# Kernel tuning notes

Hardware: AMD Instinct MI355X
Metric: run time of the kernel (lower is better)

Reference implementation:

```python
import jax, jax.numpy as jnp
import numpy as np

D = 256  # input_dim


def setup_inputs() -> dict:
    key = jax.random.key(0)
    ks = jax.random.split(key, 10)
    s = 1.0 / np.sqrt(D)  # torch Linear init scale (uniform bound)
    desc0 = jax.random.normal(ks[0], (4, 4096, D), dtype=jnp.float32)
    desc1 = jax.random.normal(ks[1], (4, 4096, D), dtype=jnp.float32)
    def lin(kw, kb):
        W = jax.random.uniform(kw, (D, D), jnp.float32, -s, s)
        b = jax.random.uniform(kb, (D,), jnp.float32, -s, s)
        return W, b
    Wq, bq = lin(ks[2], ks[3])
    Wk, bk = lin(ks[4], ks[5])
    Wv, bv = lin(ks[6], ks[7])
    Wo, bo = lin(ks[8], ks[9])
    return {"desc0": desc0, "desc1": desc1,
            "Wq": Wq, "bq": bq, "Wk": Wk, "bk": bk,
            "Wv": Wv, "bv": bv, "Wo": Wo, "bo": bo}


def reference(desc0, desc1, Wq, bq, Wk, bk, Wv, bv, Wo, bo):
    # torch Linear: y = x @ W.T + b
    q = desc0 @ Wq.T + bq                      # [B, N0, D]
    k = desc1 @ Wk.T + bk                      # [B, N1, D]
    v = desc1 @ Wv.T + bv                      # [B, N1, D]
    scale = 1.0 / jnp.sqrt(jnp.asarray(q.shape[-1], q.dtype))
    attn = jnp.einsum('bqd,bkd->bqk', q, k) * scale  # [B, N0, N1]
    weights = jax.nn.softmax(attn, axis=-1)
    out = jnp.einsum('bqk,bkd->bqd', weights, v)     # [B, N0, D]
    return out @ Wo.T + bo
```

## Files before the change

kernel.cpp:

```cpp
#include <hip/hip_runtime.h>


typedef __attribute__((ext_vector_type(8))) __bf16 bf16x8;
typedef __attribute__((ext_vector_type(4))) float f32x4;
typedef __attribute__((ext_vector_type(16))) float f32x16;
typedef __attribute__((ext_vector_type(4))) unsigned int u32x4;
typedef __attribute__((ext_vector_type(2))) unsigned int u32x2;
typedef __attribute__((ext_vector_type(4))) unsigned short us16x4;

__device__ __forceinline__ unsigned short f2bf(float f) {
  unsigned u = __builtin_bit_cast(unsigned, f);
  u += 0x7FFFu + ((u >> 16) & 1u);
  return (unsigned short)(u >> 16);
}
__device__ __forceinline__ unsigned pk2(float a, float b) {
  return (unsigned)f2bf(a) | ((unsigned)f2bf(b) << 16);
}
__device__ __forceinline__ unsigned cvtpk(float lo, float hi) {
  unsigned r;
  asm("v_cvt_pk_bf16_f32 %0, %1, %2" : "=v"(r) : "v"(lo), "v"(hi));
  return r;
}
__device__ __forceinline__ float bf2f(unsigned short s) {
  return __builtin_bit_cast(float, ((unsigned)s) << 16);
}
__device__ __forceinline__ int swz4(int r) { return (r ^ (r >> 2)) & 3; }
__device__ __forceinline__ bf16x8 ldbf16(const void* p) {
  return __builtin_bit_cast(bf16x8, *(const u32x4*)p);
}
__device__ __forceinline__ f32x4 mfma16(bf16x8 a, bf16x8 b, f32x4 c) {
  return __builtin_amdgcn_mfma_f32_16x16x32_bf16(a, b, c, 0, 0, 0);
}
__device__ __forceinline__ f32x16 mfma32(bf16x8 a, bf16x8 b, f32x16 c) {
  return __builtin_amdgcn_mfma_f32_32x32x16_bf16(a, b, c, 0, 0, 0);
}
__device__ __forceinline__ void gld16(void* lds, const void* gsrc) {
  __builtin_amdgcn_global_load_lds(
      (const __attribute__((address_space(1))) unsigned int*)gsrc,
      (__attribute__((address_space(3))) unsigned int*)lds, 16, 0, 0);
}

template <int IN_MODE, int MODE>
__global__ __launch_bounds__(256, 4) void proj_k(const void* __restrict__ Ain,
                                                 const float* __restrict__ W,
                                                 const float* __restrict__ bias,
                                                 void* __restrict__ Cout,
                                                 const float* __restrict__ lwA) {
  __shared__ __align__(16) unsigned short Al[2][64 * 32];
  __shared__ __align__(16) unsigned short Wl[2][64 * 32];
  __shared__ float biasl[64];
  const int tid = threadIdx.x;
  const int w = tid >> 6, l = tid & 63, g = l >> 4, c = l & 15;
  const int mt = blockIdx.x & 255, nq = blockIdx.x >> 8;
  const int row0 = mt * 64, n0 = nq * 64;
  if (tid < 64) biasl[tid] = bias[n0 + tid];

  const int sr = tid >> 2, seg = tid & 3;
  const int ssw = swz4(sr);

  float ainv = 1.f;
  if (IN_MODE >= 2) {
    const int grow = row0 + sr;
    float lt = lwA[grow];
    if (IN_MODE == 2) lt += lwA[16384 + grow];
    ainv = 1.f / lt;
  }

  {
    if (IN_MODE == 1) {
      const unsigned short* ap = (const unsigned short*)Ain + (size_t)(row0 + sr) * 256 + seg * 8;
      *(u32x4*)&Al[0][sr * 32 + ((seg ^ ssw) << 3)] = *(const u32x4*)ap;
    } else if (IN_MODE >= 2) {
      const unsigned short* ap = (const unsigned short*)Ain + (size_t)(row0 + sr) * 256 + seg * 8;
      u32x4 a0 = *(const u32x4*)ap, v;
      u32x4 a1 = (IN_MODE == 2) ? *(const u32x4*)(ap + 4194304) : a0;
#pragma unroll
      for (int i = 0; i < 4; ++i) {
        float lo = bf2f((unsigned short)(a0[i] & 0xFFFF));
        float hi = bf2f((unsigned short)(a0[i] >> 16));
        if (IN_MODE == 2) {
          lo += bf2f((unsigned short)(a1[i] & 0xFFFF));
          hi += bf2f((unsigned short)(a1[i] >> 16));
        }
        v[i] = pk2(lo * ainv, hi * ainv);
      }
      *(u32x4*)&Al[0][sr * 32 + ((seg ^ ssw) << 3)] = v;
    } else {
      const float* ap = (const float*)Ain + (size_t)(row0 + sr) * 256 + seg * 8;
      float4 x = *(const float4*)ap, y = *(const float4*)(ap + 4);
      u32x4 v; v[0] = pk2(x.x, x.y); v[1] = pk2(x.z, x.w); v[2] = pk2(y.x, y.y); v[3] = pk2(y.z, y.w);
      *(u32x4*)&Al[0][sr * 32 + ((seg ^ ssw) << 3)] = v;
    }
    const float* wp = W + (size_t)(n0 + sr) * 256 + seg * 8;
    float4 x = *(const float4*)wp, y = *(const float4*)(wp + 4);
    u32x4 v; v[0] = pk2(x.x, x.y); v[1] = pk2(x.z, x.w); v[2] = pk2(y.x, y.y); v[3] = pk2(y.z, y.w);
    *(u32x4*)&Wl[0][sr * 32 + ((seg ^ ssw) << 3)] = v;
  }
  __syncthreads();

  f32x4 acc[4];
#pragma unroll
  for (int jt = 0; jt < 4; ++jt) acc[jt] = (f32x4){0.f, 0.f, 0.f, 0.f};

#pragma unroll 1
  for (int ch = 0; ch < 8; ++ch) {
    const int cur = ch & 1;
    const bool pre = (ch + 1 < 8);
    float4 ax, ay, wx, wy; u32x4 abv, abv2;
    if (pre) {
      const int ko = (ch + 1) * 32 + seg * 8;
      if (IN_MODE == 1) {
        abv = *(const u32x4*)((const unsigned short*)Ain + (size_t)(row0 + sr) * 256 + ko);
      } else if (IN_MODE >= 2) {
        const unsigned short* ap = (const unsigned short*)Ain + (size_t)(row0 + sr) * 256 + ko;
        abv = *(const u32x4*)ap;
        if (IN_MODE == 2) abv2 = *(const u32x4*)(ap + 4194304);
      } else {
        const float* ap = (const float*)Ain + (size_t)(row0 + sr) * 256 + ko;
        ax = *(const float4*)ap; ay = *(const float4*)(ap + 4);
      }
      const float* wp = W + (size_t)(n0 + sr) * 256 + ko;
      wx = *(const float4*)wp; wy = *(const float4*)(wp + 4);
    }
    const int ra = w * 16 + c;
    bf16x8 af = ldbf16(&Al[cur][ra * 32 + ((g ^ swz4(ra)) << 3)]);
#pragma unroll
    for (int jt = 0; jt < 4; ++jt) {
      const int j = jt * 16 + c;
      bf16x8 bfr = ldbf16(&Wl[cur][j * 32 + ((g ^ swz4(j)) << 3)]);
      acc[jt] = mfma16(af, bfr, acc[jt]);
    }
    if (pre) {
      u32x4 v;
      if (IN_MODE == 1) v = abv;
      else if (IN_MODE >= 2) {
#pragma unroll
        for (int i = 0; i < 4; ++i) {
          float lo = bf2f((unsigned short)(abv[i] & 0xFFFF));
          float hi = bf2f((unsigned short)(abv[i] >> 16));
          if (IN_MODE == 2) {
            lo += bf2f((unsigned short)(abv2[i] & 0xFFFF));
            hi += bf2f((unsigned short)(abv2[i] >> 16));
          }
          v[i] = pk2(lo * ainv, hi * ainv);
        }
      } else {
        v[0] = pk2(ax.x, ax.y); v[1] = pk2(ax.z, ax.w); v[2] = pk2(ay.x, ay.y); v[3] = pk2(ay.z, ay.w);
      }
      *(u32x4*)&Al[1 - cur][sr * 32 + ((seg ^ ssw) << 3)] = v;
      u32x4 vw; vw[0] = pk2(wx.x, wx.y); vw[1] = pk2(wx.z, wx.w); vw[2] = pk2(wy.x, wy.y); vw[3] = pk2(wy.z, wy.w);
      *(u32x4*)&Wl[1 - cur][sr * 32 + ((seg ^ ssw) << 3)] = vw;
    }
    __syncthreads();
  }

#pragma unroll
  for (int jt = 0; jt < 4; ++jt) {
    const int col = n0 + jt * 16 + c;
    const float bv = biasl[jt * 16 + c];
    const int rloc = w * 16 + (g << 2);
    if (MODE == 0) {
      unsigned short* q = (unsigned short*)Cout;
#pragma unroll
      for (int r = 0; r < 4; ++r)
        q[(size_t)(row0 + rloc + r) * 256 + col] = f2bf(acc[jt][r] + bv);
    } else if (MODE == 1) {
      unsigned short* vt = (unsigned short*)Cout;
      const int n = row0 + rloc;
      const int b = n >> 12, nl = n & 4095;
      us16x4 pk;
      pk[0] = f2bf(acc[jt][0] + bv); pk[1] = f2bf(acc[jt][1] + bv);
      pk[2] = f2bf(acc[jt][2] + bv); pk[3] = f2bf(acc[jt][3] + bv);
      *(us16x4*)(vt + (size_t)b * 1048576 + (size_t)(nl >> 6) * 16384 + col * 64 + (nl & 63)) = pk;
    } else {
      float* o = (float*)Cout;
#pragma unroll
      for (int r = 0; r < 4; ++r)
        o[(size_t)(row0 + rloc + r) * 256 + col] = acc[jt][r] + bv;
    }
  }
}

template <int NS>
__global__ __launch_bounds__(512, 2) void attn_k(const unsigned short* __restrict__ qg,
                                                 const unsigned short* __restrict__ kg,
                                                 const unsigned short* __restrict__ vg,
                                                 unsigned short* __restrict__ part,
                                                 float* __restrict__ lw) {
  __shared__ __align__(16) unsigned char smem[148480];
  const int tid = threadIdx.x, w = tid >> 6, l = tid & 63;
  const int l31 = l & 31, h5 = l >> 5;
  const int qt = w >> 1, hf = w & 1;
  const int dh = w >> 1, qh = w & 1;
  const int bid = blockIdx.x;
  const int b4 = bid & 3;
  const int s = (NS == 2) ? ((bid >> 2) & 1) : 0;
  const int qtl = (NS == 2) ? (bid >> 3) : (bid >> 2);
  const int q0 = qtl * 128;
  const int NT = (NS == 2) ? 32 : 64;

  const unsigned short* kb = kg + (size_t)b4 * 1048576 + (size_t)s * 524288;
  const unsigned short* vb = vg + (size_t)b4 * 1048576 + (size_t)s * 32 * 16384;

  bf16x8 qf[16];
  {
    const unsigned short* qp = qg + ((size_t)b4 * 4096 + q0 + qt * 32 + l31) * 256;
#pragma unroll
    for (int kst = 0; kst < 16; ++kst) qf[kst] = ldbf16(qp + kst * 16 + h5 * 8);
  }

  f32x16 o[4];
#pragma unroll
  for (int d = 0; d < 4; ++d)
#pragma unroll
    for (int r = 0; r < 16; ++r) o[d][r] = 0.f;
  float l_run = 0.f;

  int goffK[4], goffV[4];
#pragma unroll
  for (int i = 0; i < 4; ++i) {
    const int sl = i * 512 + tid;
    const int kk = sl >> 5, ch = sl & 31;
    goffK[i] = kk * 256 + ((ch ^ (kk & 31)) << 3);
    const int r = sl >> 4, p16 = sl & 15;
    const int x = p16 ^ (r & 15);
    goffV[i] = (2 * r + (x >> 3)) * 64 + ((x & 7) << 3);
  }
#define STAGE(buf, t1)                                                                   \
  {                                                                                      \
    const unsigned short* _ks = kb + (size_t)(t1) * 16384;                               \
    const unsigned short* _vs = vb + (size_t)(t1) * 16384;                               \
    _Pragma("unroll") for (int i = 0; i < 4; ++i)                                        \
        gld16(smem + (buf) * 32768 + i * 8192 + w * 1024, _ks + goffK[i]);               \
    _Pragma("unroll") for (int i = 0; i < 4; ++i)                                        \
        gld16(smem + 65536 + (buf) * 32768 + i * 8192 + w * 1024, _vs + goffV[i]);       \
  }

  STAGE(0, 0);
  __syncthreads();

  const float alpha = 0.09016844f;
  unsigned char* Pq = smem + 131072 + qt * 4096;
  const int kkr = hf * 32 + l31;

#pragma unroll 1
  for (int t = 0; t < NT; ++t) {
    const int cur = t & 1;
    if (t + 1 < NT) STAGE(1 - cur, t + 1);

    const unsigned char* Kc = smem + cur * 32768 + kkr * 512;
    f32x16 sa, sb;
#pragma unroll
    for (int r = 0; r < 16; ++r) { sa[r] = 0.f; sb[r] = 0.f; }
    __builtin_amdgcn_s_setprio(1);
#pragma unroll
    for (int kst = 0; kst < 16; ++kst) {
      bf16x8 kf = ldbf16(Kc + (((kst * 2 + h5) ^ l31) << 4));
      if (kst & 1) sb = mfma32(kf, qf[kst], sb);
      else         sa = mfma32(kf, qf[kst], sa);
    }
    __builtin_amdgcn_s_setprio(0);

    float p[16];
#pragma unroll
    for (int r = 0; r < 16; ++r) p[r] = exp2f((sa[r] + sb[r]) * alpha);
    float ls = ((p[0] + p[1]) + (p[2] + p[3])) + ((p[4] + p[5]) + (p[6] + p[7])) +
               (((p[8] + p[9]) + (p[10] + p[11])) + ((p[12] + p[13]) + (p[14] + p[15])));
    ls += __shfl_xor(ls, 32);
    l_run += ls;

    unsigned u[8];
#pragma unroll
    for (int i = 0; i < 8; ++i) u[i] = cvtpk(p[2 * i], p[2 * i + 1]);
#pragma unroll
    for (int j = 0; j < 4; ++j) {
      u32x2 dv; dv[0] = u[2 * j]; dv[1] = u[2 * j + 1];
      *(u32x2*)(Pq + l31 * 128 + (((j + 4 * hf) ^ (l31 & 7)) << 4) + h5 * 8) = dv;
    }

    asm volatile("s_waitcnt lgkmcnt(0)\n\ts_barrier" ::: "memory");
    __builtin_amdgcn_sched_barrier(0);

    const unsigned char* Vc = smem + 65536 + cur * 32768;
    bf16x8 va[8];
#pragma unroll
    for (int dd = 0; dd < 2; ++dd) {
      const int dm = dh * 64 + dd * 32 + l31;
      const int rr = dm >> 1;
      const unsigned char* Vr = Vc + rr * 256;
      const int xb = (dm & 1) * 8;
#pragma unroll
      for (int kst = 0; kst < 4; ++kst)
        va[dd * 4 + kst] = ldbf16(Vr + (((xb + kst * 2 + h5) ^ (rr & 15)) << 4));
    }
    __builtin_amdgcn_s_setprio(1);
#pragma unroll
    for (int qq = 0; qq < 2; ++qq) {
      const unsigned char* Pr = smem + 131072 + (qh * 2 + qq) * 4096;
      bf16x8 pb[4];
#pragma unroll
      for (int kst = 0; kst < 4; ++kst)
        pb[kst] = ldbf16(Pr + l31 * 128 + (((kst * 2 + h5) ^ (l31 & 7)) << 4));
#pragma unroll
      for (int dd = 0; dd < 2; ++dd)
#pragma unroll
        for (int kst = 0; kst < 4; ++kst)
          o[dd * 2 + qq] = mfma32(va[dd * 4 + kst], pb[kst], o[dd * 2 + qq]);
    }
    __builtin_amdgcn_s_setprio(0);

    __syncthreads();
  }
#undef STAGE

  float* Lb = (float*)(smem + 147456);
  if (l < 32) Lb[(qt * 2 + hf) * 32 + l31] = l_run;
  __syncthreads();

  unsigned char* T = smem + w * 16384;
#pragma unroll
  for (int dd = 0; dd < 2; ++dd)
#pragma unroll
    for (int qq = 0; qq < 2; ++qq)
#pragma unroll
      for (int rg = 0; rg < 4; ++rg) {
        f32x4 wv;
        wv[0] = o[dd * 2 + qq][4 * rg + 0]; wv[1] = o[dd * 2 + qq][4 * rg + 1];
        wv[2] = o[dd * 2 + qq][4 * rg + 2]; wv[3] = o[dd * 2 + qq][4 * rg + 3];
        const int qloc = qq * 32 + l31;
        const int c16 = dd * 8 + rg * 2 + h5;
        *(f32x4*)(T + qloc * 256 + ((c16 ^ (qloc & 15)) << 4)) = wv;
      }
  asm volatile("s_waitcnt lgkmcnt(0)" ::: "memory");
  __builtin_amdgcn_sched_barrier(0);
  {
    const int qloc = l;
    f32x4 rv[16];
#pragma unroll
    for (int c16 = 0; c16 < 16; ++c16)
      rv[c16] = *(const f32x4*)(T + qloc * 256 + ((c16 ^ (qloc & 15)) << 4));
    unsigned short* op = part + (size_t)s * 4194304 +
                         ((size_t)b4 * 4096 + q0 + qh * 64 + qloc) * 256 + dh * 64;
#pragma unroll
    for (int i = 0; i < 8; ++i) {
      u32x4 ov;
      ov[0] = pk2(rv[2 * i][0], rv[2 * i][1]);
      ov[1] = pk2(rv[2 * i][2], rv[2 * i][3]);
      ov[2] = pk2(rv[2 * i + 1][0], rv[2 * i + 1][1]);
      ov[3] = pk2(rv[2 * i + 1][2], rv[2 * i + 1][3]);
      *(u32x4*)(op + i * 8) = ov;
    }
  }
  if (hf == 0 && l < 32) {
    const float lt = Lb[(qt * 2) * 32 + l31] + Lb[(qt * 2 + 1) * 32 + l31];
    lw[(size_t)s * 16384 + (size_t)b4 * 4096 + q0 + qt * 32 + l31] = lt;
  }
}

extern "C" void kernel_launch(void* const* d_in, const int* in_sizes, int n_in,
                              void* d_out, int out_size, void* d_ws, size_t ws_size,
                              hipStream_t stream) {
  (void)in_sizes; (void)n_in; (void)out_size;
  const float* desc0 = (const float*)d_in[0];
  const float* desc1 = (const float*)d_in[1];
  const float* Wq = (const float*)d_in[2];
  const float* bq = (const float*)d_in[3];
  const float* Wk = (const float*)d_in[4];
  const float* bk = (const float*)d_in[5];
  const float* Wv = (const float*)d_in[6];
  const float* bv = (const float*)d_in[7];
  const float* Wo = (const float*)d_in[8];
  const float* bo = (const float*)d_in[9];

  unsigned char* ws = (unsigned char*)d_ws;
  unsigned short* qw = (unsigned short*)(ws);
  unsigned short* kw = (unsigned short*)(ws + 8388608);
  unsigned short* vw = (unsigned short*)(ws + 16777216);
  unsigned short* part = (unsigned short*)(ws + 25165824);
  float* lwp = (float*)(ws + 41943040);

  const bool two = (ws_size >= 42008576ull);

  proj_k<0, 0><<<1024, 256, 0, stream>>>(desc0, Wq, bq, qw, nullptr);
  proj_k<0, 0><<<1024, 256, 0, stream>>>(desc1, Wk, bk, kw, nullptr);
  proj_k<0, 1><<<1024, 256, 0, stream>>>(desc1, Wv, bv, vw, nullptr);
  if (two) {
    attn_k<2><<<256, 512, 0, stream>>>(qw, kw, vw, part, lwp);
    proj_k<2, 2><<<1024, 256, 0, stream>>>(part, Wo, bo, (float*)d_out, lwp);
  } else {
    lwp = (float*)(ws + 33554432);
    attn_k<1><<<128, 512, 0, stream>>>(qw, kw, vw, part, lwp);
    proj_k<3, 2><<<1024, 256, 0, stream>>>(part, Wo, bo, (float*)d_out, lwp);
  }
}
```

Before: 132.5 us.

## Pre-convert weights to bf16 and compute full-width 64x256 projection tiles per block

Adds a small kernel that converts all four weight matrices to bf16 once, so each projection block streams bf16 weights through async global-to-LDS loads instead of converting fp32 weights itself. Each projection block now covers 64 rows by all 256 output columns with 512 threads, so the A tile is loaded and converted once rather than four times across column blocks. The epilogue writes packed vector stores, using swapped MFMA operands for the row-major outputs. The changes cost an extra launch, a larger LDS footprint per block, and the removal of the LDS swizzle, which may cause bank conflicts.

```diff
diff --git a/kernel.cpp b/kernel.cpp
--- a/kernel.cpp
+++ b/kernel.cpp
@@ -24,7 +24,6 @@
 __device__ __forceinline__ float bf2f(unsigned short s) {
   return __builtin_bit_cast(float, ((unsigned)s) << 16);
 }
-__device__ __forceinline__ int swz4(int r) { return (r ^ (r >> 2)) & 3; }
 __device__ __forceinline__ bf16x8 ldbf16(const void* p) {
   return __builtin_bit_cast(bf16x8, *(const u32x4*)p);
 }
@@ -40,145 +39,160 @@
       (__attribute__((address_space(3))) unsigned int*)lds, 16, 0, 0);
 }
 
+__global__ __launch_bounds__(256, 8) void wconv_k(const float* __restrict__ w0,
+                                                  const float* __restrict__ w1,
+                                                  const float* __restrict__ w2,
+                                                  const float* __restrict__ w3,
+                                                  unsigned short* __restrict__ out) {
+  const int b = blockIdx.x, t = threadIdx.x;
+  const int wi = b >> 5;
+  const float* src = wi == 0 ? w0 : wi == 1 ? w1 : wi == 2 ? w2 : w3;
+  const int idx = ((b & 31) * 256 + t) * 8;
+  float4 x = *(const float4*)(src + idx), y = *(const float4*)(src + idx + 4);
+  u32x4 v;
+  v[0] = pk2(x.x, x.y); v[1] = pk2(x.z, x.w);
+  v[2] = pk2(y.x, y.y); v[3] = pk2(y.z, y.w);
+  *(u32x4*)(out + (size_t)wi * 65536 + idx) = v;
+}
+
 template <int IN_MODE, int MODE>
-__global__ __launch_bounds__(256, 4) void proj_k(const void* __restrict__ Ain,
-                                                 const float* __restrict__ W,
+__global__ __launch_bounds__(512, 2) void proj_k(const void* __restrict__ Ain,
+                                                 const unsigned short* __restrict__ Wb,
                                                  const float* __restrict__ bias,
                                                  void* __restrict__ Cout,
                                                  const float* __restrict__ lwA) {
   __shared__ __align__(16) unsigned short Al[2][64 * 32];
-  __shared__ __align__(16) unsigned short Wl[2][64 * 32];
-  __shared__ float biasl[64];
-  const int tid = threadIdx.x;
-  const int w = tid >> 6, l = tid & 63, g = l >> 4, c = l & 15;
-  const int mt = blockIdx.x & 255, nq = blockIdx.x >> 8;
-  const int row0 = mt * 64, n0 = nq * 64;
-  if (tid < 64) biasl[tid] = bias[n0 + tid];
-
-  const int sr = tid >> 2, seg = tid & 3;
-  const int ssw = swz4(sr);
-
+  __shared__ __align__(16) unsigned short Wl[2][256 * 32];
+  __shared__ float biasl[256];
+  const int tid = threadIdx.x, w = tid >> 6, l = tid & 63, g = l >> 4, c = l & 15;
+  const int rt = w >> 1, ch2 = w & 1;
+  const int row0 = blockIdx.x * 64;
+  if (tid < 256) biasl[tid] = bias[tid];
+
+  const int arow = tid >> 3, aseg = tid & 7;
+  const int agrow = row0 + arow;
   float ainv = 1.f;
   if (IN_MODE >= 2) {
-    const int grow = row0 + sr;
-    float lt = lwA[grow];
-    if (IN_MODE == 2) lt += lwA[16384 + grow];
+    float lt = lwA[agrow];
+    if (IN_MODE == 2) lt += lwA[16384 + agrow];
     ainv = 1.f / lt;
   }
 
+#define STAGEW(buf, ch1)                                                            \
+  {                                                                                 \
+    gld16((unsigned char*)Wl[buf] + tid * 16,                                       \
+          Wb + (tid >> 2) * 256 + (ch1) * 32 + (tid & 3) * 8);                      \
+    gld16((unsigned char*)Wl[buf] + (tid + 512) * 16,                               \
+          Wb + ((tid + 512) >> 2) * 256 + (ch1) * 32 + (tid & 3) * 8);              \
+  }
+#define ACONV(dst, A4, M0, M1)                                                      \
+  {                                                                                 \
+    u32x2 _v;                                                                       \
+    if (IN_MODE == 0) { _v[0] = pk2((A4).x, (A4).y); _v[1] = pk2((A4).z, (A4).w); } \
+    else {                                                                          \
+      float _e0 = bf2f((unsigned short)((M0)[0] & 0xFFFF));                         \
+      float _e1 = bf2f((unsigned short)((M0)[0] >> 16));                            \
+      float _e2 = bf2f((unsigned short)((M0)[1] & 0xFFFF));                         \
+      float _e3 = bf2f((unsigned short)((M0)[1] >> 16));                            \
+      if (IN_MODE == 2) {                                                           \
+        _e0 += bf2f((unsigned short)((M1)[0] & 0xFFFF));                            \
+        _e1 += bf2f((unsigned short)((M1)[0] >> 16));                               \
+        _e2 += bf2f((unsigned short)((M1)[1] & 0xFFFF));                            \
+        _e3 += bf2f((unsigned short)((M1)[1] >> 16));                               \
+      }                                                                             \
+      _v[0] = pk2(_e0 * ainv, _e1 * ainv); _v[1] = pk2(_e2 * ainv, _e3 * ainv);     \
+    }                                                                               \
+    *(u32x2*)(dst) = _v;                                                            \
+  }
+
   {
-    if (IN_MODE == 1) {
-      const unsigned short* ap = (const unsigned short*)Ain + (size_t)(row0 + sr) * 256 + seg * 8;
-      *(u32x4*)&Al[0][sr * 32 + ((seg ^ ssw) << 3)] = *(const u32x4*)ap;
-    } else if (IN_MODE >= 2) {
-      const unsigned short* ap = (const unsigned short*)Ain + (size_t)(row0 + sr) * 256 + seg * 8;
-      u32x4 a0 = *(const u32x4*)ap, v;
-      u32x4 a1 = (IN_MODE == 2) ? *(const u32x4*)(ap + 4194304) : a0;
-#pragma unroll
-      for (int i = 0; i < 4; ++i) {
-        float lo = bf2f((unsigned short)(a0[i] & 0xFFFF));
-        float hi = bf2f((unsigned short)(a0[i] >> 16));
-        if (IN_MODE == 2) {
-          lo += bf2f((unsigned short)(a1[i] & 0xFFFF));
-          hi += bf2f((unsigned short)(a1[i] >> 16));
-        }
-        v[i] = pk2(lo * ainv, hi * ainv);
-      }
-      *(u32x4*)&Al[0][sr * 32 + ((seg ^ ssw) << 3)] = v;
+    STAGEW(0, 0);
+    float4 a4; u32x2 m0, m1;
+    if (IN_MODE == 0) {
+      a4 = *(const float4*)((const float*)Ain + (size_t)agrow * 256 + aseg * 4);
     } else {
-      const float* ap = (const float*)Ain + (size_t)(row0 + sr) * 256 + seg * 8;
-      float4 x = *(const float4*)ap, y = *(const float4*)(ap + 4);
-      u32x4 v; v[0] = pk2(x.x, x.y); v[1] = pk2(x.z, x.w); v[2] = pk2(y.x, y.y); v[3] = pk2(y.z, y.w);
-      *(u32x4*)&Al[0][sr * 32 + ((seg ^ ssw) << 3)] = v;
-    }
-    const float* wp = W + (size_t)(n0 + sr) * 256 + seg * 8;
-    float4 x = *(const float4*)wp, y = *(const float4*)(wp + 4);
-    u32x4 v; v[0] = pk2(x.x, x.y); v[1] = pk2(x.z, x.w); v[2] = pk2(y.x, y.y); v[3] = pk2(y.z, y.w);
-    *(u32x4*)&Wl[0][sr * 32 + ((seg ^ ssw) << 3)] = v;
-  }
-  __syncthreads();
-
-  f32x4 acc[4];
-#pragma unroll
-  for (int jt = 0; jt < 4; ++jt) acc[jt] = (f32x4){0.f, 0.f, 0.f, 0.f};
+      const unsigned short* p0 = (const unsigned short*)Ain + (size_t)agrow * 256 + aseg * 4;
+      m0 = *(const u32x2*)p0;
+      if (IN_MODE == 2) m1 = *(const u32x2*)(p0 + 4194304);
+    }
+    ACONV(&Al[0][arow * 32 + aseg * 4], a4, m0, m1);
+    __syncthreads();
+  }
+
+  f32x4 acc[8];
+#pragma unroll
+  for (int ct = 0; ct < 8; ++ct) acc[ct] = (f32x4){0.f, 0.f, 0.f, 0.f};
 
 #pragma unroll 1
   for (int ch = 0; ch < 8; ++ch) {
     const int cur = ch & 1;
     const bool pre = (ch + 1 < 8);
-    float4 ax, ay, wx, wy; u32x4 abv, abv2;
+    float4 a4; u32x2 m0, m1;
     if (pre) {
-      const int ko = (ch + 1) * 32 + seg * 8;
-      if (IN_MODE == 1) {
-        abv = *(const u32x4*)((const unsigned short*)Ain + (size_t)(row0 + sr) * 256 + ko);
-      } else if (IN_MODE >= 2) {
-        const unsigned short* ap = (const unsigned short*)Ain + (size_t)(row0 + sr) * 256 + ko;
-        abv = *(const u32x4*)ap;
-        if (IN_MODE == 2) abv2 = *(const u32x4*)(ap + 4194304);
+      const int ko = (ch + 1) * 32 + aseg * 4;
+      if (IN_MODE == 0) {
+        a4 = *(const float4*)((const float*)Ain + (size_t)agrow * 256 + ko);
       } else {
-        const float* ap = (const float*)Ain + (size_t)(row0 + sr) * 256 + ko;
-        ax = *(const float4*)ap; ay = *(const float4*)(ap + 4);
+        const unsigned short* p0 = (const unsigned short*)Ain + (size_t)agrow * 256 + ko;
+        m0 = *(const u32x2*)p0;
+        if (IN_MODE == 2) m1 = *(const u32x2*)(p0 + 4194304);
       }
-      const float* wp = W + (size_t)(n0 + sr) * 256 + ko;
-      wx = *(const float4*)wp; wy = *(const float4*)(wp + 4);
-    }
-    const int ra = w * 16 + c;
-    bf16x8 af = ldbf16(&Al[cur][ra * 32 + ((g ^ swz4(ra)) << 3)]);
-#pragma unroll
-    for (int jt = 0; jt < 4; ++jt) {
-      const int j = jt * 16 + c;
-      bf16x8 bfr = ldbf16(&Wl[cur][j * 32 + ((g ^ swz4(j)) << 3)]);
-      acc[jt] = mfma16(af, bfr, acc[jt]);
-    }
-    if (pre) {
-      u32x4 v;
-      if (IN_MODE == 1) v = abv;
-      else if (IN_MODE >= 2) {
-#pragma unroll
-        for (int i = 0; i < 4; ++i) {
-          float lo = bf2f((unsigned short)(abv[i] & 0xFFFF));
-          float hi = bf2f((unsigned short)(abv[i] >> 16));
-          if (IN_MODE == 2) {
-            lo += bf2f((unsigned short)(abv2[i] & 0xFFFF));
-            hi += bf2f((unsigned short)(abv2[i] >> 16));
-          }
-          v[i] = pk2(lo * ainv, hi * ainv);
-        }
-      } else {
-        v[0] = pk2(ax.x, ax.y); v[1] = pk2(ax.z, ax.w); v[2] = pk2(ay.x, ay.y); v[3] = pk2(ay.z, ay.w);
-      }
-      *(u32x4*)&Al[1 - cur][sr * 32 + ((seg ^ ssw) << 3)] = v;
-      u32x4 vw; vw[0] = pk2(wx.x, wx.y); vw[1] = pk2(wx.z, wx.w); vw[2] = pk2(wy.x, wy.y); vw[3] = pk2(wy.z, wy.w);
-      *(u32x4*)&Wl[1 - cur][sr * 32 + ((seg ^ ssw) << 3)] = vw;
-    }
+      STAGEW(1 - cur, ch + 1);
+    }
+    bf16x8 af = ldbf16(&Al[cur][(rt * 16 + c) * 32 + g * 8]);
+#pragma unroll
+    for (int ct = 0; ct < 8; ++ct) {
+      const int j = ch2 * 128 + ct * 16 + c;
+      bf16x8 wf = ldbf16(&Wl[cur][j * 32 + g * 8]);
+      if (MODE == 1) acc[ct] = mfma16(af, wf, acc[ct]);
+      else           acc[ct] = mfma16(wf, af, acc[ct]);
+    }
+    if (pre) ACONV(&Al[1 - cur][arow * 32 + aseg * 4], a4, m0, m1);
     __syncthreads();
   }
 
-#pragma unroll
-  for (int jt = 0; jt < 4; ++jt) {
-    const int col = n0 + jt * 16 + c;
-    const float bv = biasl[jt * 16 + c];
-    const int rloc = w * 16 + (g << 2);
-    if (MODE == 0) {
-      unsigned short* q = (unsigned short*)Cout;
-#pragma unroll
-      for (int r = 0; r < 4; ++r)
-        q[(size_t)(row0 + rloc + r) * 256 + col] = f2bf(acc[jt][r] + bv);
-    } else if (MODE == 1) {
-      unsigned short* vt = (unsigned short*)Cout;
-      const int n = row0 + rloc;
-      const int b = n >> 12, nl = n & 4095;
+  if (MODE == 1) {
+    unsigned short* vt = (unsigned short*)Cout;
+    const int b = row0 >> 12, nb = (row0 & 4095) >> 6;
+    const int nloc = rt * 16 + g * 4;
+#pragma unroll
+    for (int ct = 0; ct < 8; ++ct) {
+      const int col = ch2 * 128 + ct * 16 + c;
+      const float bv = biasl[col];
       us16x4 pk;
-      pk[0] = f2bf(acc[jt][0] + bv); pk[1] = f2bf(acc[jt][1] + bv);
-      pk[2] = f2bf(acc[jt][2] + bv); pk[3] = f2bf(acc[jt][3] + bv);
-      *(us16x4*)(vt + (size_t)b * 1048576 + (size_t)(nl >> 6) * 16384 + col * 64 + (nl & 63)) = pk;
-    } else {
-      float* o = (float*)Cout;
-#pragma unroll
-      for (int r = 0; r < 4; ++r)
-        o[(size_t)(row0 + rloc + r) * 256 + col] = acc[jt][r] + bv;
-    }
-  }
+      pk[0] = f2bf(acc[ct][0] + bv); pk[1] = f2bf(acc[ct][1] + bv);
+      pk[2] = f2bf(acc[ct][2] + bv); pk[3] = f2bf(acc[ct][3] + bv);
+      *(us16x4*)(vt + (size_t)b * 1048576 + (size_t)nb * 16384 + col * 64 + nloc) = pk;
+    }
+  } else if (MODE == 0) {
+    unsigned short* q = (unsigned short*)Cout;
+    const int row = row0 + rt * 16 + c;
+#pragma unroll
+    for (int ct = 0; ct < 8; ++ct) {
+      const int col = ch2 * 128 + ct * 16 + g * 4;
+      us16x4 pk;
+      pk[0] = f2bf(acc[ct][0] + biasl[col + 0]);
+      pk[1] = f2bf(acc[ct][1] + biasl[col + 1]);
+      pk[2] = f2bf(acc[ct][2] + biasl[col + 2]);
+      pk[3] = f2bf(acc[ct][3] + biasl[col + 3]);
+      *(us16x4*)(q + (size_t)row * 256 + col) = pk;
+    }
+  } else {
+    float* o = (float*)Cout;
+    const int row = row0 + rt * 16 + c;
+#pragma unroll
+    for (int ct = 0; ct < 8; ++ct) {
+      const int col = ch2 * 128 + ct * 16 + g * 4;
+      float4 ov;
+      ov.x = acc[ct][0] + biasl[col + 0];
+      ov.y = acc[ct][1] + biasl[col + 1];
+      ov.z = acc[ct][2] + biasl[col + 2];
+      ov.w = acc[ct][3] + biasl[col + 3];
+      *(float4*)(o + (size_t)row * 256 + col) = ov;
+    }
+  }
+#undef STAGEW
+#undef ACONV
 }
 
 template <int NS>
@@ -377,19 +391,27 @@
   unsigned short* kw = (unsigned short*)(ws + 8388608);
   unsigned short* vw = (unsigned short*)(ws + 16777216);
   unsigned short* part = (unsigned short*)(ws + 25165824);
-  float* lwp = (float*)(ws + 41943040);
-
-  const bool two = (ws_size >= 42008576ull);
-
-  proj_k<0, 0><<<1024, 256, 0, stream>>>(desc0, Wq, bq, qw, nullptr);
-  proj_k<0, 0><<<1024, 256, 0, stream>>>(desc1, Wk, bk, kw, nullptr);
-  proj_k<0, 1><<<1024, 256, 0, stream>>>(desc1, Wv, bv, vw, nullptr);
+
+  const bool two = (ws_size >= 42598400ull);
+  float* lwp;
+  unsigned short* wbf;
+  if (two) {
+    lwp = (float*)(ws + 41943040);
+    wbf = (unsigned short*)(ws + 42074112);
+  } else {
+    lwp = (float*)(ws + 33554432);
+    wbf = (unsigned short*)(ws + 33685504);
+  }
+
+  wconv_k<<<128, 256, 0, stream>>>(Wq, Wk, Wv, Wo, wbf);
+  proj_k<0, 0><<<256, 512, 0, stream>>>(desc0, wbf + 0 * 65536, bq, qw, nullptr);
+  proj_k<0, 0><<<256, 512, 0, stream>>>(desc1, wbf + 1 * 65536, bk, kw, nullptr);
+  proj_k<0, 1><<<256, 512, 0, stream>>>(desc1, wbf + 2 * 65536, bv, vw, nullptr);
   if (two) {
     attn_k<2><<<256, 512, 0, stream>>>(qw, kw, vw, part, lwp);
-    proj_k<2, 2><<<1024, 256, 0, stream>>>(part, Wo, bo, (float*)d_out, lwp);
+    proj_k<2, 2><<<256, 512, 0, stream>>>(part, wbf + 3 * 65536, bo, (float*)d_out, lwp);
   } else {
-    lwp = (float*)(ws + 33554432);
     attn_k<1><<<128, 512, 0, stream>>>(qw, kw, vw, part, lwp);
-    proj_k<3, 2><<<1024, 256, 0, stream>>>(part, Wo, bo, (float*)d_out, lwp);
-  }
-}
+    proj_k<3, 2><<<256, 512, 0, stream>>>(part, wbf + 3 * 65536, bo, (float*)d_out, lwp);
+  }
+}
```

Measured after the change: 138.7 us. 1.05x slower.

## Split attention warps into QK producer and PV consumer roles with skewed pipeline

Applied to the files above, without the earlier changes.

The attention kernel now gives its warps two roles. Four warps compute QK scores and exponentials for a 32-key tile, and four warps run the P·V MFMAs for the previous tile one step behind. K tiles are double-buffered, V tiles triple-buffered and P double-buffered in shared memory, with the key tile halved and the tile count doubled. The aim is to overlap softmax math with PV tensor work and drop the mid-iteration barrier. In exchange, consumer warps hold twice the accumulator registers and the unused IN_MODE==1 paths are removed from the projection kernel.

```diff
diff --git a/kernel.cpp b/kernel.cpp
--- a/kernel.cpp
+++ b/kernel.cpp
@@ -67,10 +67,7 @@
   }
 
   {
-    if (IN_MODE == 1) {
-      const unsigned short* ap = (const unsigned short*)Ain + (size_t)(row0 + sr) * 256 + seg * 8;
-      *(u32x4*)&Al[0][sr * 32 + ((seg ^ ssw) << 3)] = *(const u32x4*)ap;
-    } else if (IN_MODE >= 2) {
+    if (IN_MODE >= 2) {
       const unsigned short* ap = (const unsigned short*)Ain + (size_t)(row0 + sr) * 256 + seg * 8;
       u32x4 a0 = *(const u32x4*)ap, v;
       u32x4 a1 = (IN_MODE == 2) ? *(const u32x4*)(ap + 4194304) : a0;
@@ -109,9 +106,7 @@
     float4 ax, ay, wx, wy; u32x4 abv, abv2;
     if (pre) {
       const int ko = (ch + 1) * 32 + seg * 8;
-      if (IN_MODE == 1) {
-        abv = *(const u32x4*)((const unsigned short*)Ain + (size_t)(row0 + sr) * 256 + ko);
-      } else if (IN_MODE >= 2) {
+      if (IN_MODE >= 2) {
         const unsigned short* ap = (const unsigned short*)Ain + (size_t)(row0 + sr) * 256 + ko;
         abv = *(const u32x4*)ap;
         if (IN_MODE == 2) abv2 = *(const u32x4*)(ap + 4194304);
@@ -132,8 +127,7 @@
     }
     if (pre) {
       u32x4 v;
-      if (IN_MODE == 1) v = abv;
-      else if (IN_MODE >= 2) {
+      if (IN_MODE >= 2) {
 #pragma unroll
         for (int i = 0; i < 4; ++i) {
           float lo = bf2f((unsigned short)(abv[i] & 0xFFFF));
@@ -187,173 +181,168 @@
                                                  const unsigned short* __restrict__ vg,
                                                  unsigned short* __restrict__ part,
                                                  float* __restrict__ lw) {
-  __shared__ __align__(16) unsigned char smem[148480];
+  __shared__ __align__(16) unsigned char smem[131072];
   const int tid = threadIdx.x, w = tid >> 6, l = tid & 63;
   const int l31 = l & 31, h5 = l >> 5;
-  const int qt = w >> 1, hf = w & 1;
-  const int dh = w >> 1, qh = w & 1;
+  const bool prod = (w < 4);
+  const int role = w & 3;
   const int bid = blockIdx.x;
   const int b4 = bid & 3;
   const int s = (NS == 2) ? ((bid >> 2) & 1) : 0;
   const int qtl = (NS == 2) ? (bid >> 3) : (bid >> 2);
   const int q0 = qtl * 128;
-  const int NT = (NS == 2) ? 32 : 64;
+  const int NT = (NS == 2) ? 64 : 128;
 
   const unsigned short* kb = kg + (size_t)b4 * 1048576 + (size_t)s * 524288;
   const unsigned short* vb = vg + (size_t)b4 * 1048576 + (size_t)s * 32 * 16384;
 
   bf16x8 qf[16];
-  {
-    const unsigned short* qp = qg + ((size_t)b4 * 4096 + q0 + qt * 32 + l31) * 256;
+  if (prod) {
+    const unsigned short* qp = qg + ((size_t)b4 * 4096 + q0 + role * 32 + l31) * 256;
 #pragma unroll
     for (int kst = 0; kst < 16; ++kst) qf[kst] = ldbf16(qp + kst * 16 + h5 * 8);
   }
-
-  f32x16 o[4];
-#pragma unroll
-  for (int d = 0; d < 4; ++d)
-#pragma unroll
-    for (int r = 0; r < 16; ++r) o[d][r] = 0.f;
+  f32x16 o[8];
+  if (!prod) {
+#pragma unroll
+    for (int i = 0; i < 8; ++i)
+#pragma unroll
+      for (int r = 0; r < 16; ++r) o[i][r] = 0.f;
+  }
   float l_run = 0.f;
 
-  int goffK[4], goffV[4];
-#pragma unroll
-  for (int i = 0; i < 4; ++i) {
+  int gK[2], gV[2];
+#pragma unroll
+  for (int i = 0; i < 2; ++i) {
     const int sl = i * 512 + tid;
     const int kk = sl >> 5, ch = sl & 31;
-    goffK[i] = kk * 256 + ((ch ^ (kk & 31)) << 3);
-    const int r = sl >> 4, p16 = sl & 15;
-    const int x = p16 ^ (r & 15);
-    goffV[i] = (2 * r + (x >> 3)) * 64 + ((x & 7) << 3);
-  }
-#define STAGE(buf, t1)                                                                   \
-  {                                                                                      \
-    const unsigned short* _ks = kb + (size_t)(t1) * 16384;                               \
-    const unsigned short* _vs = vb + (size_t)(t1) * 16384;                               \
-    _Pragma("unroll") for (int i = 0; i < 4; ++i)                                        \
-        gld16(smem + (buf) * 32768 + i * 8192 + w * 1024, _ks + goffK[i]);               \
-    _Pragma("unroll") for (int i = 0; i < 4; ++i)                                        \
-        gld16(smem + 65536 + (buf) * 32768 + i * 8192 + w * 1024, _vs + goffV[i]);       \
-  }
-
-  STAGE(0, 0);
+    gK[i] = kk * 256 + ((ch ^ kk) << 3);
+    const int rr = sl >> 3, cc = (sl & 7) ^ (rr & 7);
+    gV[i] = (rr * 2 + (cc >> 2)) * 64 + ((cc & 3) << 3);
+  }
+#define STAGE(t1)                                                                   \
+  {                                                                                 \
+    const int _t = (t1);                                                            \
+    const unsigned short* _ks = kb + (size_t)_t * 8192;                             \
+    const unsigned short* _vs = vb + (size_t)(_t >> 1) * 16384 + (_t & 1) * 32;     \
+    unsigned char* _kd = smem + (_t & 1) * 16384;                                   \
+    unsigned char* _vd = smem + 32768 + (_t % 3) * 16384;                           \
+    _Pragma("unroll") for (int i = 0; i < 2; ++i)                                   \
+        gld16(_kd + (i * 512 + tid) * 16, _ks + gK[i]);                             \
+    _Pragma("unroll") for (int i = 0; i < 2; ++i)                                   \
+        gld16(_vd + (i * 512 + tid) * 16, _vs + gV[i]);                             \
+  }
+#define PVSTEP(tm1)                                                                 \
+  {                                                                                 \
+    const unsigned char* Vc = smem + 32768 + ((tm1) % 3) * 16384;                   \
+    const unsigned char* Pc = smem + 81920 + ((tm1) & 1) * 8192;                    \
+    bf16x8 va[4];                                                                   \
+    _Pragma("unroll") for (int dd = 0; dd < 2; ++dd) {                              \
+      const int dm = role * 64 + dd * 32 + l31;                                     \
+      const int rr = dm >> 1;                                                       \
+      _Pragma("unroll") for (int kst = 0; kst < 2; ++kst)                           \
+          va[dd * 2 + kst] = ldbf16(Vc + rr * 128 +                                 \
+              ((((dm & 1) * 4 + kst * 2 + h5) ^ (rr & 7)) << 4));                   \
+    }                                                                               \
+    __builtin_amdgcn_s_setprio(1);                                                  \
+    _Pragma("unroll") for (int qq = 0; qq < 4; ++qq) {                              \
+      const unsigned char* Pr = Pc + qq * 2048 + l31 * 64;                          \
+      bf16x8 pb0 = ldbf16(Pr + (((0 + h5) ^ (l31 & 3)) << 4));                      \
+      bf16x8 pb1 = ldbf16(Pr + (((2 + h5) ^ (l31 & 3)) << 4));                      \
+      _Pragma("unroll") for (int dd = 0; dd < 2; ++dd) {                            \
+        o[dd * 4 + qq] = mfma32(va[dd * 2 + 0], pb0, o[dd * 4 + qq]);               \
+        o[dd * 4 + qq] = mfma32(va[dd * 2 + 1], pb1, o[dd * 4 + qq]);               \
+      }                                                                             \
+    }                                                                               \
+    __builtin_amdgcn_s_setprio(0);                                                  \
+  }
+
+  STAGE(0);
   __syncthreads();
 
   const float alpha = 0.09016844f;
-  unsigned char* Pq = smem + 131072 + qt * 4096;
-  const int kkr = hf * 32 + l31;
 
 #pragma unroll 1
   for (int t = 0; t < NT; ++t) {
-    const int cur = t & 1;
-    if (t + 1 < NT) STAGE(1 - cur, t + 1);
-
-    const unsigned char* Kc = smem + cur * 32768 + kkr * 512;
-    f32x16 sa, sb;
-#pragma unroll
-    for (int r = 0; r < 16; ++r) { sa[r] = 0.f; sb[r] = 0.f; }
-    __builtin_amdgcn_s_setprio(1);
-#pragma unroll
-    for (int kst = 0; kst < 16; ++kst) {
-      bf16x8 kf = ldbf16(Kc + (((kst * 2 + h5) ^ l31) << 4));
-      if (kst & 1) sb = mfma32(kf, qf[kst], sb);
-      else         sa = mfma32(kf, qf[kst], sa);
-    }
-    __builtin_amdgcn_s_setprio(0);
-
-    float p[16];
-#pragma unroll
-    for (int r = 0; r < 16; ++r) p[r] = exp2f((sa[r] + sb[r]) * alpha);
-    float ls = ((p[0] + p[1]) + (p[2] + p[3])) + ((p[4] + p[5]) + (p[6] + p[7])) +
-               (((p[8] + p[9]) + (p[10] + p[11])) + ((p[12] + p[13]) + (p[14] + p[15])));
-    ls += __shfl_xor(ls, 32);
-    l_run += ls;
-
-    unsigned u[8];
-#pragma unroll
-    for (int i = 0; i < 8; ++i) u[i] = cvtpk(p[2 * i], p[2 * i + 1]);
-#pragma unroll
-    for (int j = 0; j < 4; ++j) {
-      u32x2 dv; dv[0] = u[2 * j]; dv[1] = u[2 * j + 1];
-      *(u32x2*)(Pq + l31 * 128 + (((j + 4 * hf) ^ (l31 & 7)) << 4) + h5 * 8) = dv;
-    }
-
-    asm volatile("s_waitcnt lgkmcnt(0)\n\ts_barrier" ::: "memory");
+    if (t + 1 < NT) STAGE(t + 1);
+    if (prod) {
+      const unsigned char* Kc = smem + (t & 1) * 16384 + l31 * 512;
+      f32x16 sa, sb;
+#pragma unroll
+      for (int r = 0; r < 16; ++r) { sa[r] = 0.f; sb[r] = 0.f; }
+      __builtin_amdgcn_s_setprio(1);
+#pragma unroll
+      for (int kst = 0; kst < 16; ++kst) {
+        bf16x8 kf = ldbf16(Kc + (((kst * 2 + h5) ^ l31) << 4));
+        if (kst & 1) sb = mfma32(kf, qf[kst], sb);
+        else         sa = mfma32(kf, qf[kst], sa);
+      }
+      __builtin_amdgcn_s_setprio(0);
+      float p[16];
+#pragma unroll
+      for (int r = 0; r < 16; ++r) p[r] = exp2f((sa[r] + sb[r]) * alpha);
+      float ls = ((p[0] + p[1]) + (p[2] + p[3])) + ((p[4] + p[5]) + (p[6] + p[7])) +
+                 (((p[8] + p[9]) + (p[10] + p[11])) + ((p[12] + p[13]) + (p[14] + p[15])));
+      ls += __shfl_xor(ls, 32);
+      l_run += ls;
+      unsigned u[8];
+#pragma unroll
+      for (int i = 0; i < 8; ++i) u[i] = cvtpk(p[2 * i], p[2 * i + 1]);
+      unsigned char* Pq = smem + 81920 + (t & 1) * 8192 + role * 2048 + l31 * 64;
+#pragma unroll
+      for (int j = 0; j < 4; ++j) {
+        u32x2 dv; dv[0] = u[2 * j]; dv[1] = u[2 * j + 1];
+        *(u32x2*)(Pq + ((j ^ (l31 & 3)) << 4) + h5 * 8) = dv;
+      }
+    } else if (t > 0) {
+      PVSTEP(t - 1);
+    }
+    __syncthreads();
+  }
+  if (!prod) PVSTEP(NT - 1);
+#undef STAGE
+#undef PVSTEP
+
+  if (prod && l < 32)
+    lw[(size_t)s * 16384 + (size_t)b4 * 4096 + q0 + role * 32 + l31] = l_run;
+  __syncthreads();
+
+  if (!prod) {
+    unsigned char* T = smem + role * 32768;
+#pragma unroll
+    for (int dd = 0; dd < 2; ++dd)
+#pragma unroll
+      for (int qq = 0; qq < 4; ++qq)
+#pragma unroll
+        for (int rg = 0; rg < 4; ++rg) {
+          f32x4 wv;
+          wv[0] = o[dd * 4 + qq][4 * rg + 0]; wv[1] = o[dd * 4 + qq][4 * rg + 1];
+          wv[2] = o[dd * 4 + qq][4 * rg + 2]; wv[3] = o[dd * 4 + qq][4 * rg + 3];
+          const int qr = qq * 32 + l31;
+          const int c16 = dd * 8 + rg * 2 + h5;
+          *(f32x4*)(T + qr * 256 + ((c16 ^ (qr & 15)) << 4)) = wv;
+        }
+    asm volatile("s_waitcnt lgkmcnt(0)" ::: "memory");
     __builtin_amdgcn_sched_barrier(0);
-
-    const unsigned char* Vc = smem + 65536 + cur * 32768;
-    bf16x8 va[8];
-#pragma unroll
-    for (int dd = 0; dd < 2; ++dd) {
-      const int dm = dh * 64 + dd * 32 + l31;
-      const int rr = dm >> 1;
-      const unsigned char* Vr = Vc + rr * 256;
-      const int xb = (dm & 1) * 8;
-#pragma unroll
-      for (int kst = 0; kst < 4; ++kst)
-        va[dd * 4 + kst] = ldbf16(Vr + (((xb + kst * 2 + h5) ^ (rr & 15)) << 4));
-    }
-    __builtin_amdgcn_s_setprio(1);
-#pragma unroll
-    for (int qq = 0; qq < 2; ++qq) {
-      const unsigned char* Pr = smem + 131072 + (qh * 2 + qq) * 4096;
-      bf16x8 pb[4];
-#pragma unroll
-      for (int kst = 0; kst < 4; ++kst)
-        pb[kst] = ldbf16(Pr + l31 * 128 + (((kst * 2 + h5) ^ (l31 & 7)) << 4));
-#pragma unroll
-      for (int dd = 0; dd < 2; ++dd)
-#pragma unroll
-        for (int kst = 0; kst < 4; ++kst)
-          o[dd * 2 + qq] = mfma32(va[dd * 4 + kst], pb[kst], o[dd * 2 + qq]);
-    }
-    __builtin_amdgcn_s_setprio(0);
-
-    __syncthreads();
-  }
-#undef STAGE
-
-  float* Lb = (float*)(smem + 147456);
-  if (l < 32) Lb[(qt * 2 + hf) * 32 + l31] = l_run;
-  __syncthreads();
-
-  unsigned char* T = smem + w * 16384;
-#pragma unroll
-  for (int dd = 0; dd < 2; ++dd)
-#pragma unroll
-    for (int qq = 0; qq < 2; ++qq)
-#pragma unroll
-      for (int rg = 0; rg < 4; ++rg) {
-        f32x4 wv;
-        wv[0] = o[dd * 2 + qq][4 * rg + 0]; wv[1] = o[dd * 2 + qq][4 * rg + 1];
-        wv[2] = o[dd * 2 + qq][4 * rg + 2]; wv[3] = o[dd * 2 + qq][4 * rg + 3];
-        const int qloc = qq * 32 + l31;
-        const int c16 = dd * 8 + rg * 2 + h5;
-        *(f32x4*)(T + qloc * 256 + ((c16 ^ (qloc & 15)) << 4)) = wv;
-      }
-  asm volatile("s_waitcnt lgkmcnt(0)" ::: "memory");
-  __builtin_amdgcn_sched_barrier(0);
-  {
-    const int qloc = l;
-    f32x4 rv[16];
-#pragma unroll
-    for (int c16 = 0; c16 < 16; ++c16)
-      rv[c16] = *(const f32x4*)(T + qloc * 256 + ((c16 ^ (qloc & 15)) << 4));
-    unsigned short* op = part + (size_t)s * 4194304 +
-                         ((size_t)b4 * 4096 + q0 + qh * 64 + qloc) * 256 + dh * 64;
-#pragma unroll
-    for (int i = 0; i < 8; ++i) {
-      u32x4 ov;
-      ov[0] = pk2(rv[2 * i][0], rv[2 * i][1]);
-      ov[1] = pk2(rv[2 * i][2], rv[2 * i][3]);
-      ov[2] = pk2(rv[2 * i + 1][0], rv[2 * i + 1][1]);
-      ov[3] = pk2(rv[2 * i + 1][2], rv[2 * i + 1][3]);
-      *(u32x4*)(op + i * 8) = ov;
-    }
-  }
-  if (hf == 0 && l < 32) {
-    const float lt = Lb[(qt * 2) * 32 + l31] + Lb[(qt * 2 + 1) * 32 + l31];
-    lw[(size_t)s * 16384 + (size_t)b4 * 4096 + q0 + qt * 32 + l31] = lt;
+#pragma unroll
+    for (int half = 0; half < 2; ++half) {
+      const int qr = half * 64 + l;
+      f32x4 rv[16];
+#pragma unroll
+      for (int c16 = 0; c16 < 16; ++c16)
+        rv[c16] = *(const f32x4*)(T + qr * 256 + ((c16 ^ (qr & 15)) << 4));
+      unsigned short* op = part + (size_t)s * 4194304 +
+                           ((size_t)b4 * 4096 + q0 + qr) * 256 + role * 64;
+#pragma unroll
+      for (int i = 0; i < 8; ++i) {
+        u32x4 ov;
+        ov[0] = pk2(rv[2 * i][0], rv[2 * i][1]);
+        ov[1] = pk2(rv[2 * i][2], rv[2 * i][3]);
+        ov[2] = pk2(rv[2 * i + 1][0], rv[2 * i + 1][1]);
+        ov[3] = pk2(rv[2 * i + 1][2], rv[2 * i + 1][3]);
+        *(u32x4*)(op + i * 8) = ov;
+      }
+    }
   }
 }
 
```

Result: slower. 171.2 us (+29.2%).
